# Optimization experiments

Measured on AMD Instinct MI355X. Metric: run time of the kernel, lower is better.

The kernel has to match this reference:

```python
import jax, jax.numpy as jnp
import numpy as np

SCALING = 128.0 / 64.0   # alpha / r
DT = 0.1
TAU_MIN = 0.1
TAU_MAX = 10.0
ADAPT_STEPS = 3


def setup_inputs() -> dict:
    key = jax.random.key(0)
    ks = jax.random.split(key, 6)
    B, S, D, O, R = 4, 4096, 4096, 4096, 64
    x = jax.random.normal(ks[0], (B, S, D), dtype=jnp.float32)
    # kaiming_uniform-ish init for lora_A; lora_B nominally zeros in torch but
    # we use small random values so the dynamics/matmul are non-trivial.
    lora_A = jax.random.normal(ks[1], (R, D), dtype=jnp.float32) * (1.0 / np.sqrt(D))
    lora_B = jax.random.normal(ks[2], (O, R), dtype=jnp.float32) * 0.02
    hidden_B = jnp.zeros((O, R), dtype=jnp.float32)
    W_gate = jax.random.normal(ks[3], (R, 2 * R), dtype=jnp.float32) * (1.0 / np.sqrt(2 * R))
    b_gate = jnp.zeros((R,), dtype=jnp.float32)
    W_tau = jax.random.normal(ks[4], (R, 2 * R), dtype=jnp.float32) * (1.0 / np.sqrt(2 * R))
    b_tau = jnp.zeros((R,), dtype=jnp.float32)
    return {"x": x, "lora_A": lora_A, "lora_B": lora_B, "hidden_B": hidden_B,
            "W_gate": W_gate, "b_gate": b_gate, "W_tau": W_tau, "b_tau": b_tau}


def _liquid_step(h, target, W_gate, b_gate, W_tau, b_tau):
    # Batched over all out_features rows at once: h, target are [O, r].
    inp = jnp.concatenate([target, h], axis=-1)               # [O, 2r]
    f = jax.nn.sigmoid(inp @ W_gate.T + b_gate)               # gate f(x, B, t)
    tau = TAU_MIN + (TAU_MAX - TAU_MIN) * jax.nn.sigmoid(inp @ W_tau.T + b_tau)
    a = 1.0 / tau + f                                         # effective decay rate
    decay = jnp.exp(-a * DT)
    # closed-form integration of dh/dt = -a*h + f*target over dt
    return h * decay + (f / a) * target * (1.0 - decay)


def reference(x, lora_A, lora_B, hidden_B, W_gate, b_gate, W_tau, b_tau):
    # Liquid dynamics update (torch runs this under no_grad on a buffer).
    target = lora_B                                           # [O, r]
    def body(_, h):
        return _liquid_step(h, target, W_gate, b_gate, W_tau, b_tau)
    hidden_new = jax.lax.fori_loop(0, ADAPT_STEPS, body, hidden_B)
    hidden_new = jax.lax.stop_gradient(hidden_new)
    # straight-through: value from liquid state, gradient from lora_B
    B_eff = hidden_new + lora_B - jax.lax.stop_gradient(lora_B)  # [O, r]
    # (B_eff @ lora_A @ x^T)^T == x @ A^T @ B_eff^T
    lora_out = jnp.einsum('bsi,ri,or->bso', x, lora_A, B_eff, optimize=True)
    return lora_out * SCALING
```

## Files before the change

kernel.cpp:

```cpp
#include <hip/hip_runtime.h>


typedef __attribute__((ext_vector_type(8))) short short8;
typedef __attribute__((ext_vector_type(4))) short short4_t;
typedef __attribute__((ext_vector_type(4))) float f32x4;

static __device__ __forceinline__ unsigned short f2bf(float f) {
    unsigned int x;
    __builtin_memcpy(&x, &f, 4);
    x += 0x7fffu + ((x >> 16) & 1);
    return (unsigned short)(x >> 16);
}
static __device__ __forceinline__ float bf2f(unsigned short u) {
    unsigned int x = ((unsigned int)u) << 16;
    float f;
    __builtin_memcpy(&f, &x, 4);
    return f;
}

__global__ __launch_bounds__(256) void liquid_kernel(
    const float* __restrict__ loraB,
    const float* __restrict__ hiddenB,
    const float* __restrict__ Wg,
    const float* __restrict__ bg,
    const float* __restrict__ Wt,
    const float* __restrict__ bt,
    unsigned short* __restrict__ beff)
{
    __shared__ __align__(16) float inp[16][132];
    const int tid = threadIdx.x;
    const int row = tid >> 4;
    const int cg  = tid & 15;
    const int orow = blockIdx.x * 16 + row;
    const int c0 = cg * 4;

    float tgt[4], h[4], bgv[4], btv[4];
#pragma unroll
    for (int i = 0; i < 4; ++i) {
        tgt[i] = loraB[orow * 64 + c0 + i];
        h[i]   = hiddenB[orow * 64 + c0 + i];
        bgv[i] = bg[c0 + i];
        btv[i] = bt[c0 + i];
        inp[row][c0 + i] = tgt[i];
    }
    for (int step = 0; step < 3; ++step) {
#pragma unroll
        for (int i = 0; i < 4; ++i) inp[row][64 + c0 + i] = h[i];
        __syncthreads();
        float dg[4], dt_[4];
#pragma unroll
        for (int c = 0; c < 4; ++c) { dg[c] = bgv[c]; dt_[c] = btv[c]; }
        for (int k = 0; k < 128; k += 4) {
            f32x4 iv = *(f32x4*)&inp[row][k];
#pragma unroll
            for (int c = 0; c < 4; ++c) {
                f32x4 wgv = *(const f32x4*)&Wg[(c0 + c) * 128 + k];
                f32x4 wtv = *(const f32x4*)&Wt[(c0 + c) * 128 + k];
                dg[c]  += iv[0]*wgv[0] + iv[1]*wgv[1] + iv[2]*wgv[2] + iv[3]*wgv[3];
                dt_[c] += iv[0]*wtv[0] + iv[1]*wtv[1] + iv[2]*wtv[2] + iv[3]*wtv[3];
            }
        }
#pragma unroll
        for (int c = 0; c < 4; ++c) {
            float f   = 1.f / (1.f + __expf(-dg[c]));
            float tau = 0.1f + 9.9f / (1.f + __expf(-dt_[c]));
            float a   = 1.f / tau + f;
            float dec = __expf(-a * 0.1f);
            h[c] = h[c] * dec + (f / a) * tgt[c] * (1.f - dec);
        }
        __syncthreads();
    }
#pragma unroll
    for (int i = 0; i < 4; ++i)
        beff[orow * 64 + c0 + i] = f2bf(h[i]);
}

__global__ __launch_bounds__(512) void lora_gemm_kernel(
    const float* __restrict__ x,
    const float* __restrict__ loraA,
    const unsigned short* __restrict__ beff,
    float* __restrict__ out)
{
    __shared__ __align__(16) union {
        struct { unsigned short xs[64 * 136]; unsigned short as[64 * 136]; } p1;
        struct { unsigned short bs[128 * 72]; float bounce[64 * 132]; } p2;
    } sm;
    __shared__ __align__(16) unsigned short tsh[64 * 72];
    __shared__ __align__(16) unsigned short tsl[64 * 72];

    const int tid  = threadIdx.x;
    const int lane = tid & 63;
    const int w    = tid >> 6;
    const int q    = lane >> 4;
    const int ln   = lane & 15;
    const int m0   = blockIdx.x * 64;
    const int ms   = (w >> 1) * 16;
    const int nb   = (w & 1) * 32;

    f32x4 acc0 = (f32x4){0.f, 0.f, 0.f, 0.f};
    f32x4 acc1 = (f32x4){0.f, 0.f, 0.f, 0.f};

    for (int k0 = 0; k0 < 4096; k0 += 128) {
        f32x4 xv[4], av[4];
#pragma unroll
        for (int i = 0; i < 4; ++i) {
            int c = tid + i * 512;
            int r = c >> 5, c4 = (c & 31) * 4;
            xv[i] = *(const f32x4*)&x[(size_t)(m0 + r) * 4096 + k0 + c4];
            av[i] = *(const f32x4*)&loraA[(size_t)r * 4096 + k0 + c4];
        }
        __syncthreads();
#pragma unroll
        for (int i = 0; i < 4; ++i) {
            int c = tid + i * 512;
            int r = c >> 5, c4 = (c & 31) * 4;
            short4_t xb, ab;
#pragma unroll
            for (int j = 0; j < 4; ++j) {
                xb[j] = (short)f2bf(xv[i][j]);
                ab[j] = (short)f2bf(av[i][j]);
            }
            *(short4_t*)&sm.p1.xs[r * 136 + c4] = xb;
            *(short4_t*)&sm.p1.as[r * 136 + c4] = ab;
        }
        __syncthreads();
#pragma unroll
        for (int kk = 0; kk < 128; kk += 32) {
            short8 af = *(short8*)&sm.p1.xs[(ms + ln) * 136 + kk + q * 8];
            short8 b0 = *(short8*)&sm.p1.as[(nb + ln) * 136 + kk + q * 8];
            short8 b1 = *(short8*)&sm.p1.as[(nb + 16 + ln) * 136 + kk + q * 8];
            acc0 = __builtin_amdgcn_mfma_f32_16x16x32_bf16(af, b0, acc0, 0, 0, 0);
            acc1 = __builtin_amdgcn_mfma_f32_16x16x32_bf16(af, b1, acc1, 0, 0, 0);
        }
    }
#pragma unroll
    for (int r = 0; r < 4; ++r) {
        float v0 = acc0[r], v1 = acc1[r];
        unsigned short h0 = f2bf(v0), h1 = f2bf(v1);
        tsh[(ms + q * 4 + r) * 72 + nb + ln]      = h0;
        tsl[(ms + q * 4 + r) * 72 + nb + ln]      = f2bf(v0 - bf2f(h0));
        tsh[(ms + q * 4 + r) * 72 + nb + 16 + ln] = h1;
        tsl[(ms + q * 4 + r) * 72 + nb + 16 + ln] = f2bf(v1 - bf2f(h1));
    }

    const int nb2 = (w & 1) * 64;
    for (int o0 = 0; o0 < 4096; o0 += 128) {
        short8 bv[2];
#pragma unroll
        for (int i = 0; i < 2; ++i) {
            int c = tid + i * 512;
            int r = c >> 3, c8 = (c & 7) * 8;
            bv[i] = *(const short8*)&beff[(size_t)(o0 + r) * 64 + c8];
        }
        __syncthreads();
#pragma unroll
        for (int i = 0; i < 2; ++i) {
            int c = tid + i * 512;
            int r = c >> 3, c8 = (c & 7) * 8;
            *(short8*)&sm.p2.bs[r * 72 + c8] = bv[i];
        }
        __syncthreads();
        f32x4 a2[4];
#pragma unroll
        for (int t = 0; t < 4; ++t) a2[t] = (f32x4){0.f, 0.f, 0.f, 0.f};
#pragma unroll
        for (int kk = 0; kk < 64; kk += 32) {
            short8 ah = *(short8*)&tsh[(ms + ln) * 72 + kk + q * 8];
            short8 al = *(short8*)&tsl[(ms + ln) * 72 + kk + q * 8];
#pragma unroll
            for (int t = 0; t < 4; ++t) {
                short8 bf = *(short8*)&sm.p2.bs[(nb2 + t * 16 + ln) * 72 + kk + q * 8];
                a2[t] = __builtin_amdgcn_mfma_f32_16x16x32_bf16(ah, bf, a2[t], 0, 0, 0);
                a2[t] = __builtin_amdgcn_mfma_f32_16x16x32_bf16(al, bf, a2[t], 0, 0, 0);
            }
        }
#pragma unroll
        for (int t = 0; t < 4; ++t)
#pragma unroll
            for (int r = 0; r < 4; ++r)
                sm.p2.bounce[(ms + q * 4 + r) * 132 + nb2 + t * 16 + ln] =
                    a2[t][r] * 2.0f;
        __syncthreads();
#pragma unroll
        for (int i = 0; i < 4; ++i) {
            int c = tid + i * 512;
            int r = c >> 5, c4 = (c & 31) * 4;
            *(f32x4*)&out[(size_t)(m0 + r) * 4096 + o0 + c4] =
                *(f32x4*)&sm.p2.bounce[r * 132 + c4];
        }
    }
}

extern "C" void kernel_launch(void* const* d_in, const int* in_sizes, int n_in,
                              void* d_out, int out_size, void* d_ws, size_t ws_size,
                              hipStream_t stream) {
    const float* x       = (const float*)d_in[0];
    const float* loraA   = (const float*)d_in[1];
    const float* loraB   = (const float*)d_in[2];
    const float* hiddenB = (const float*)d_in[3];
    const float* Wg      = (const float*)d_in[4];
    const float* bg      = (const float*)d_in[5];
    const float* Wt      = (const float*)d_in[6];
    const float* bt      = (const float*)d_in[7];
    float* out = (float*)d_out;
    unsigned short* beff = (unsigned short*)d_ws;

    hipLaunchKernelGGL(liquid_kernel, dim3(256), dim3(256), 0, stream,
                       loraB, hiddenB, Wg, bg, Wt, bt, beff);
    hipLaunchKernelGGL(lora_gemm_kernel, dim3(256), dim3(512), 0, stream,
                       x, loraA, beff, out);
}
```

Before: 611.0 us.

## Halve GEMM row tile, preconvert lora_A to bf16, prefetch next tiles into registers

The liquid kernel now also converts lora_A to bf16 once into workspace, so the GEMM blocks no longer each reload and convert fp32 A. The GEMM row tile shrinks from 64 to 32, doubling the grid to 512 blocks to improve CU occupancy, and each of the 8 waves owns one 16x16 output tile. Global loads for the next K or O chunk are issued before the shared-memory store and MFMA work to overlap latency. The cost is that each block still rereads the full A and B_eff matrices, so that cached traffic doubles in total, and the extra prefetch registers may raise register pressure.

```diff
diff --git a/kernel.cpp b/kernel.cpp
--- a/kernel.cpp
+++ b/kernel.cpp
@@ -25,8 +25,19 @@
     const float* __restrict__ bg,
     const float* __restrict__ Wt,
     const float* __restrict__ bt,
-    unsigned short* __restrict__ beff)
+    const float* __restrict__ loraA,
+    unsigned short* __restrict__ beff,
+    unsigned short* __restrict__ abf)
 {
+    {
+        const int idx = (blockIdx.x * 256 + threadIdx.x) * 4;
+        f32x4 a = *(const f32x4*)&loraA[idx];
+        short4_t ab;
+#pragma unroll
+        for (int j = 0; j < 4; ++j) ab[j] = (short)f2bf(a[j]);
+        *(short4_t*)&abf[idx] = ab;
+    }
+
     __shared__ __align__(16) float inp[16][132];
     const int tid = threadIdx.x;
     const int row = tid >> 4;
@@ -75,119 +86,134 @@
         beff[orow * 64 + c0 + i] = f2bf(h[i]);
 }
 
-__global__ __launch_bounds__(512) void lora_gemm_kernel(
+__global__ __launch_bounds__(512, 4) void lora_gemm_kernel(
     const float* __restrict__ x,
-    const float* __restrict__ loraA,
+    const unsigned short* __restrict__ abf,
     const unsigned short* __restrict__ beff,
     float* __restrict__ out)
 {
     __shared__ __align__(16) union {
-        struct { unsigned short xs[64 * 136]; unsigned short as[64 * 136]; } p1;
-        struct { unsigned short bs[128 * 72]; float bounce[64 * 132]; } p2;
+        struct { unsigned short xs[32 * 136]; unsigned short as[64 * 136]; } p1;
+        struct { unsigned short bs[128 * 72]; float bounce[32 * 132]; } p2;
     } sm;
-    __shared__ __align__(16) unsigned short tsh[64 * 72];
-    __shared__ __align__(16) unsigned short tsl[64 * 72];
+    __shared__ __align__(16) unsigned short tsh[32 * 72];
+    __shared__ __align__(16) unsigned short tsl[32 * 72];
 
     const int tid  = threadIdx.x;
     const int lane = tid & 63;
     const int w    = tid >> 6;
     const int q    = lane >> 4;
     const int ln   = lane & 15;
-    const int m0   = blockIdx.x * 64;
-    const int ms   = (w >> 1) * 16;
-    const int nb   = (w & 1) * 32;
-
-    f32x4 acc0 = (f32x4){0.f, 0.f, 0.f, 0.f};
-    f32x4 acc1 = (f32x4){0.f, 0.f, 0.f, 0.f};
-
-    for (int k0 = 0; k0 < 4096; k0 += 128) {
-        f32x4 xv[4], av[4];
-#pragma unroll
-        for (int i = 0; i < 4; ++i) {
-            int c = tid + i * 512;
-            int r = c >> 5, c4 = (c & 31) * 4;
-            xv[i] = *(const f32x4*)&x[(size_t)(m0 + r) * 4096 + k0 + c4];
-            av[i] = *(const f32x4*)&loraA[(size_t)r * 4096 + k0 + c4];
-        }
-        __syncthreads();
-#pragma unroll
-        for (int i = 0; i < 4; ++i) {
-            int c = tid + i * 512;
-            int r = c >> 5, c4 = (c & 31) * 4;
-            short4_t xb, ab;
+    const int m0   = blockIdx.x * 32;
+    const int ms   = (w >> 2) * 16;
+    const int nc   = (w & 3) * 16;
+
+    const int xr0 = tid >> 5,        xc0 = (tid & 31) * 4;
+    const int xr1 = xr0 + 16;
+    const int ar0 = tid >> 4,        ac0 = (tid & 15) * 8;
+    const int ar1 = ar0 + 32;
+    const int br0 = tid >> 3,        bc0 = (tid & 7) * 8;
+    const int br1 = br0 + 64;
+
+    f32x4 acc = (f32x4){0.f, 0.f, 0.f, 0.f};
+
+    const float* xp0 = &x[(size_t)(m0 + xr0) * 4096 + xc0];
+    const float* xp1 = &x[(size_t)(m0 + xr1) * 4096 + xc0];
+    const unsigned short* ap0 = &abf[(size_t)ar0 * 4096 + ac0];
+    const unsigned short* ap1 = &abf[(size_t)ar1 * 4096 + ac0];
+
+    f32x4 xcur[2]; short8 acur[2];
+    xcur[0] = *(const f32x4*)xp0;
+    xcur[1] = *(const f32x4*)xp1;
+    acur[0] = *(const short8*)ap0;
+    acur[1] = *(const short8*)ap1;
+
+    for (int it = 0; it < 32; ++it) {
+        f32x4 xn[2]; short8 an[2];
+        if (it < 31) {
+            const int k = (it + 1) * 128;
+            xn[0] = *(const f32x4*)(xp0 + k);
+            xn[1] = *(const f32x4*)(xp1 + k);
+            an[0] = *(const short8*)(ap0 + k);
+            an[1] = *(const short8*)(ap1 + k);
+        }
+        __syncthreads();
+        {
+            short4_t xb0, xb1;
 #pragma unroll
             for (int j = 0; j < 4; ++j) {
-                xb[j] = (short)f2bf(xv[i][j]);
-                ab[j] = (short)f2bf(av[i][j]);
+                xb0[j] = (short)f2bf(xcur[0][j]);
+                xb1[j] = (short)f2bf(xcur[1][j]);
             }
-            *(short4_t*)&sm.p1.xs[r * 136 + c4] = xb;
-            *(short4_t*)&sm.p1.as[r * 136 + c4] = ab;
+            *(short4_t*)&sm.p1.xs[xr0 * 136 + xc0] = xb0;
+            *(short4_t*)&sm.p1.xs[xr1 * 136 + xc0] = xb1;
+            *(short8*)&sm.p1.as[ar0 * 136 + ac0] = acur[0];
+            *(short8*)&sm.p1.as[ar1 * 136 + ac0] = acur[1];
         }
         __syncthreads();
 #pragma unroll
         for (int kk = 0; kk < 128; kk += 32) {
-            short8 af = *(short8*)&sm.p1.xs[(ms + ln) * 136 + kk + q * 8];
-            short8 b0 = *(short8*)&sm.p1.as[(nb + ln) * 136 + kk + q * 8];
-            short8 b1 = *(short8*)&sm.p1.as[(nb + 16 + ln) * 136 + kk + q * 8];
-            acc0 = __builtin_amdgcn_mfma_f32_16x16x32_bf16(af, b0, acc0, 0, 0, 0);
-            acc1 = __builtin_amdgcn_mfma_f32_16x16x32_bf16(af, b1, acc1, 0, 0, 0);
+            short8 af  = *(short8*)&sm.p1.xs[(ms + ln) * 136 + kk + q * 8];
+            short8 bfv = *(short8*)&sm.p1.as[(nc + ln) * 136 + kk + q * 8];
+            acc = __builtin_amdgcn_mfma_f32_16x16x32_bf16(af, bfv, acc, 0, 0, 0);
+        }
+        if (it < 31) {
+            xcur[0] = xn[0]; xcur[1] = xn[1];
+            acur[0] = an[0]; acur[1] = an[1];
         }
     }
 #pragma unroll
     for (int r = 0; r < 4; ++r) {
-        float v0 = acc0[r], v1 = acc1[r];
-        unsigned short h0 = f2bf(v0), h1 = f2bf(v1);
-        tsh[(ms + q * 4 + r) * 72 + nb + ln]      = h0;
-        tsl[(ms + q * 4 + r) * 72 + nb + ln]      = f2bf(v0 - bf2f(h0));
-        tsh[(ms + q * 4 + r) * 72 + nb + 16 + ln] = h1;
-        tsl[(ms + q * 4 + r) * 72 + nb + 16 + ln] = f2bf(v1 - bf2f(h1));
-    }
-
-    const int nb2 = (w & 1) * 64;
-    for (int o0 = 0; o0 < 4096; o0 += 128) {
-        short8 bv[2];
-#pragma unroll
-        for (int i = 0; i < 2; ++i) {
-            int c = tid + i * 512;
-            int r = c >> 3, c8 = (c & 7) * 8;
-            bv[i] = *(const short8*)&beff[(size_t)(o0 + r) * 64 + c8];
-        }
-        __syncthreads();
-#pragma unroll
-        for (int i = 0; i < 2; ++i) {
-            int c = tid + i * 512;
-            int r = c >> 3, c8 = (c & 7) * 8;
-            *(short8*)&sm.p2.bs[r * 72 + c8] = bv[i];
-        }
-        __syncthreads();
-        f32x4 a2[4];
-#pragma unroll
-        for (int t = 0; t < 4; ++t) a2[t] = (f32x4){0.f, 0.f, 0.f, 0.f};
+        float v = acc[r];
+        unsigned short hh = f2bf(v);
+        tsh[(ms + q * 4 + r) * 72 + nc + ln] = hh;
+        tsl[(ms + q * 4 + r) * 72 + nc + ln] = f2bf(v - bf2f(hh));
+    }
+
+    const int oc = (w & 3) * 32;
+    const unsigned short* bp0 = &beff[(size_t)br0 * 64 + bc0];
+    const unsigned short* bp1 = &beff[(size_t)br1 * 64 + bc0];
+    short8 bcur[2];
+    bcur[0] = *(const short8*)bp0;
+    bcur[1] = *(const short8*)bp1;
+
+    for (int it = 0; it < 32; ++it) {
+        const int o0 = it * 128;
+        short8 bn[2];
+        if (it < 31) {
+            bn[0] = *(const short8*)(bp0 + (it + 1) * 8192);
+            bn[1] = *(const short8*)(bp1 + (it + 1) * 8192);
+        }
+        __syncthreads();
+        *(short8*)&sm.p2.bs[br0 * 72 + bc0] = bcur[0];
+        *(short8*)&sm.p2.bs[br1 * 72 + bc0] = bcur[1];
+        __syncthreads();
+        f32x4 a2[2];
+        a2[0] = (f32x4){0.f, 0.f, 0.f, 0.f};
+        a2[1] = (f32x4){0.f, 0.f, 0.f, 0.f};
 #pragma unroll
         for (int kk = 0; kk < 64; kk += 32) {
             short8 ah = *(short8*)&tsh[(ms + ln) * 72 + kk + q * 8];
             short8 al = *(short8*)&tsl[(ms + ln) * 72 + kk + q * 8];
 #pragma unroll
-            for (int t = 0; t < 4; ++t) {
-                short8 bf = *(short8*)&sm.p2.bs[(nb2 + t * 16 + ln) * 72 + kk + q * 8];
-                a2[t] = __builtin_amdgcn_mfma_f32_16x16x32_bf16(ah, bf, a2[t], 0, 0, 0);
-                a2[t] = __builtin_amdgcn_mfma_f32_16x16x32_bf16(al, bf, a2[t], 0, 0, 0);
+            for (int t = 0; t < 2; ++t) {
+                short8 bfv = *(short8*)&sm.p2.bs[(oc + t * 16 + ln) * 72 + kk + q * 8];
+                a2[t] = __builtin_amdgcn_mfma_f32_16x16x32_bf16(ah, bfv, a2[t], 0, 0, 0);
+                a2[t] = __builtin_amdgcn_mfma_f32_16x16x32_bf16(al, bfv, a2[t], 0, 0, 0);
             }
         }
 #pragma unroll
-        for (int t = 0; t < 4; ++t)
+        for (int t = 0; t < 2; ++t)
 #pragma unroll
             for (int r = 0; r < 4; ++r)
-                sm.p2.bounce[(ms + q * 4 + r) * 132 + nb2 + t * 16 + ln] =
+                sm.p2.bounce[(ms + q * 4 + r) * 132 + oc + t * 16 + ln] =
                     a2[t][r] * 2.0f;
         __syncthreads();
-#pragma unroll
-        for (int i = 0; i < 4; ++i) {
-            int c = tid + i * 512;
-            int r = c >> 5, c4 = (c & 31) * 4;
-            *(f32x4*)&out[(size_t)(m0 + r) * 4096 + o0 + c4] =
-                *(f32x4*)&sm.p2.bounce[r * 132 + c4];
-        }
+        *(f32x4*)&out[(size_t)(m0 + xr0) * 4096 + o0 + xc0] =
+            *(f32x4*)&sm.p2.bounce[xr0 * 132 + xc0];
+        *(f32x4*)&out[(size_t)(m0 + xr1) * 4096 + o0 + xc0] =
+            *(f32x4*)&sm.p2.bounce[xr1 * 132 + xc0];
+        if (it < 31) { bcur[0] = bn[0]; bcur[1] = bn[1]; }
     }
 }
 
@@ -204,9 +230,10 @@
     const float* bt      = (const float*)d_in[7];
     float* out = (float*)d_out;
     unsigned short* beff = (unsigned short*)d_ws;
+    unsigned short* abf  = beff + 4096 * 64;
 
     hipLaunchKernelGGL(liquid_kernel, dim3(256), dim3(256), 0, stream,
-                       loraB, hiddenB, Wg, bg, Wt, bt, beff);
-    hipLaunchKernelGGL(lora_gemm_kernel, dim3(256), dim3(512), 0, stream,
-                       x, loraA, beff, out);
-}
+                       loraB, hiddenB, Wg, bg, Wt, bt, loraA, beff, abf);
+    hipLaunchKernelGGL(lora_gemm_kernel, dim3(512), dim3(512), 0, stream,
+                       x, abf, beff, out);
+}
```

Result: faster. 562.9 us (-7.9%).
